# Optimization experiments

Hardware: AMD Instinct MI355X
Metric: run time of the kernel (lower is better)

The kernel has to match this reference:

```python
import jax, jax.numpy as jnp
import numpy as np

N, C, H, W = 16, 64, 128, 128
SHIFT = 1  # frozen value of torch module's random.randint(-2, 2) drawn at __init__


def setup_inputs() -> dict:
    key = jax.random.key(0)
    k1, k2, k3 = jax.random.split(key, 3)
    x = jax.random.normal(k1, (N, C, H, W), dtype=jnp.float32)
    # p_3: Conv2d(c, c, (1,5), padding=(0,2), bias=False) -> weight (C_out, C_in, 1, 5)
    w3 = jax.random.normal(k2, (C, C, 1, 5), dtype=jnp.float32) * (1.0 / np.sqrt(5.0 * C))
    # p_7: Conv2d(9c, c, 1, groups=c, bias=False) -> per output channel, 9 input channels: (C, 9)
    w7 = jax.random.normal(k3, (C, 9), dtype=jnp.float32) * (1.0 / 3.0)
    return {"x": x, "w3": w3, "w7": w7}


def reference(x, w3, w7):
    n, c, h, w = x.shape
    # t_1: F.unfold(x, (1,3), dilation=(1,2), padding=(0,2)) -> width offsets -2, 0, +2 (zero padded)
    xp = jnp.pad(x, ((0, 0), (0, 0), (0, 0), (2, 2)))
    t1 = jnp.stack([xp[..., 0:w], xp[..., 2:w + 2], xp[..., 4:w + 4]], axis=2)  # (n,c,3,h,w)
    # t_3: 1x5 conv, padding (0,2)
    t3 = jax.lax.conv_general_dilated(
        x, w3, window_strides=(1, 1), padding=[(0, 0), (2, 2)],
        dimension_numbers=("NCHW", "OIHW", "NCHW"))  # (n,c,h,w)
    # t_4: F.unfold(t1 as (n,3c,h,w), (3,1), padding=(1,0)) -> height offsets -1, 0, +1
    t1p = jnp.pad(t1, ((0, 0), (0, 0), (0, 0), (1, 1), (0, 0)))
    t4 = jnp.stack([t1p[..., 0:h, :], t1p[..., 1:h + 1, :], t1p[..., 2:h + 2, :]],
                   axis=3)  # (n, c, 3[w_off], 3[h_off], h, w)
    # t_5: roll along the W axis (dim 5)
    t5 = jnp.roll(t4, SHIFT, axis=5)
    # t_6: maximum of lhs (n,c,1,3,h,w) and rhs (n,c,3,3,h,w); lhs offset dim aligns with rhs dim 3
    t6 = jnp.maximum(t1[:, :, None, :, :, :], t5)  # (n,c,3,3,h,w)
    # t_7: grouped 1x1 conv, groups=c, 9 input channels per group -> 1 output channel
    t6f = t6.reshape(n, c, 9, h, w)
    t7 = jnp.einsum("nckhw,ck->nchw", t6f, w7)
    return t7 * t3
```

## Files before the change

### kernel.cpp

```cpp
#include <hip/hip_runtime.h>

#define NN 16
#define CC 64
#define HH 128
#define WW 128

#define LDS_STRIDE 72
#define PANEL_DW   4752
#define ROW_BYTES  19008
#define ROW_CHUNKS 1188
#define T3B_STRIDE 132

typedef __attribute__((ext_vector_type(8))) short short8;
typedef __attribute__((ext_vector_type(4))) float floatx4;

__device__ __forceinline__ short f2bf(float f) {
    union { float f; unsigned u; } v; v.f = f;
    unsigned r = v.u + 0x7fffu + ((v.u >> 16) & 1u);
    return (short)(r >> 16);
}
__device__ __forceinline__ unsigned pack2bf(float lo, float hi) {
    union { float f; unsigned u; } a, b; a.f = lo; b.f = hi;
    unsigned ra = a.u + 0x7fffu + ((a.u >> 16) & 1u);
    unsigned rb = b.u + 0x7fffu + ((b.u >> 16) & 1u);
    return (ra >> 16) | (rb & 0xffff0000u);
}
__device__ __forceinline__ float bf2f(unsigned short u) {
    union { unsigned u; float f; } v; v.u = ((unsigned)u) << 16;
    return v.f;
}
__device__ __forceinline__ void gload_lds16(const void* g, void* l) {
    __builtin_amdgcn_global_load_lds(
        (const __attribute__((address_space(1))) void*)g,
        (__attribute__((address_space(3))) void*)l, 16, 0, 0);
}

__global__ __launch_bounds__(256) void prep_w(const float* __restrict__ w3,
                                              short* __restrict__ Apk,
                                              float* __restrict__ zp) {
    int idx = blockIdx.x * 256 + threadIdx.x;
    if (idx < CC * 320) {
        int co = idx / 320;
        int kk = idx % 320;
        int mh = co >> 5, m = (co >> 4) & 1, lm = co & 15;
        int ks = kk >> 5, g = (kk >> 3) & 3, e = kk & 7;
        int tap = kk >> 6, ci = kk & 63;
        Apk[((((mh * 10 + ks) * 2 + m) * 64) + (g * 16 + lm)) * 8 + e] =
            f2bf(w3[(co * CC + ci) * 5 + tap]);
    }
    if (blockIdx.x == 0 && threadIdx.x < 64) zp[threadIdx.x] = 0.f;
}

__global__ __launch_bounds__(256, 4) void transp(const float* __restrict__ x,
                                                 short* __restrict__ xT) {
    __shared__ __align__(16) char smem[2 * ROW_BYTES];
    unsigned* xsW = (unsigned*)smem;

    const int bid = blockIdx.x;
    const int rp  = ((bid & 7) << 7) | (bid >> 3);
    const int n   = rp >> 6;
    const int h   = (rp & 63) * 2;
    const int tid = threadIdx.x;
    const int lane = tid & 63;
    const int W    = tid >> 6;

    {
        const int ri = lane >> 5;
        const int wq = lane & 31;
        unsigned* panel = xsW + ri * PANEL_DW;
        #pragma unroll
        for (int i = 0; i < 8; ++i) {
            const int cp = W * 8 + i;
            const float* b0 = x + (((size_t)(n * CC + 2 * cp)) * HH + h) * WW;
            float4 av = *(const float4*)(b0 + lane * 4);
            float4 bv = *(const float4*)(b0 + HH * WW + lane * 4);
            #pragma unroll
            for (int k = 0; k < 4; ++k) {
                int wp = wq * 4 + 2 + k;
                panel[wp * 36 + cp] = pack2bf(av[k], bv[k]);
            }
        }
        {
            int pi  = tid >> 7;
            int idx = tid & 127;
            int wpi = idx >> 5;
            int wpz = (wpi < 2) ? wpi : 128 + wpi;
            xsW[pi * PANEL_DW + wpz * 36 + (idx & 31)] = 0u;
        }
    }
    __syncthreads();

    const size_t rowb = (size_t)(n * HH + h) * ROW_BYTES;
    #pragma unroll
    for (int pi = 0; pi < 2; ++pi) {
        short8* dst = (short8*)((char*)xT + rowb + (size_t)pi * ROW_BYTES);
        const short8* src = (const short8*)(smem + pi * ROW_BYTES);
        #pragma unroll
        for (int i = 0; i < 5; ++i) {
            int c = tid + 256 * i;
            if (c < ROW_CHUNKS) dst[c] = src[c];
        }
    }
}

__global__ __launch_bounds__(256, 6) void fused(const short* __restrict__ xT,
                                                const short* __restrict__ Apk,
                                                const float* __restrict__ x,
                                                const float* __restrict__ w7,
                                                const float* __restrict__ zp,
                                                float* __restrict__ out) {
    __shared__ __align__(16) char smem[19456];
    const short* panel = (const short*)smem;
    short*       t3b  = (short*)smem;

    const int bid = blockIdx.x;
    const int nh  = ((bid & 7) << 8) | (bid >> 3);
    const int n   = nh >> 7;
    const int h   = nh & (HH - 1);
    const int tid = threadIdx.x;
    const int lane = tid & 63;
    const int W    = tid >> 6;

    {
        const char* grow = (const char*)xT + (size_t)(n * HH + h) * ROW_BYTES;
        #pragma unroll
        for (int k2 = 0; k2 < 5; ++k2) {
            int base = (k2 * 4 + W) * 1024;
            if (base < ROW_BYTES) {
                int goff = base + lane * 16;
                if (goff > ROW_BYTES - 16) goff = ROW_BYTES - 16;
                gload_lds16(grow + goff, smem + base);
            }
        }
    }
    __syncthreads();

    const int lm = lane & 15;
    const int g  = lane >> 4;
    const int mh = W >> 1;
    const int wh = W & 1;

    floatx4 acc[2][4];
    #pragma unroll
    for (int m = 0; m < 2; ++m)
        #pragma unroll
        for (int j = 0; j < 4; ++j) acc[m][j] = (floatx4){0.f, 0.f, 0.f, 0.f};

    for (int ks = 0; ks < 10; ++ks) {
        const int kbase = ks * 32 + g * 8;
        const int tap   = kbase >> 6;
        const int cib   = kbase & 63;

        const short* ab = Apk + (((mh * 10 + ks) * 2) * 64 + lane) * 8;
        short8 a0 = *(const short8*)ab;
        short8 a1 = *(const short8*)(ab + 64 * 8);
        #pragma unroll
        for (int j = 0; j < 4; ++j) {
            int wp = (wh * 4 + j) * 16 + lm + tap;
            short8 b = *(const short8*)&panel[wp * LDS_STRIDE + cib];
            acc[0][j] = __builtin_amdgcn_mfma_f32_16x16x32_bf16(a0, b, acc[0][j], 0, 0, 0);
            acc[1][j] = __builtin_amdgcn_mfma_f32_16x16x32_bf16(a1, b, acc[1][j], 0, 0, 0);
        }
    }
    __syncthreads();

    #pragma unroll
    for (int m = 0; m < 2; ++m)
        #pragma unroll
        for (int j = 0; j < 4; ++j)
            #pragma unroll
            for (int r = 0; r < 4; ++r) {
                int co = (mh * 2 + m) * 16 + g * 4 + r;
                int w  = (wh * 4 + j) * 16 + lm;
                t3b[co * T3B_STRIDE + w] = f2bf(acc[m][j][r]);
            }

    const int w0   = (tid & 31) * 4;
    const int chi  = tid >> 5;
    const int lq31 = lane & 31;
    const bool isw = (lq31 == 0);
    const bool ise = (lq31 == 31);
    const int src31 = lane | 31;
    const int lsrc  = isw ? lane : lane - 1;
    const int rsrc  = ise ? lane : lane + 1;

    const float* pr[3]; int sr[3];
    const float* xb0 = x + (((size_t)(n * CC + chi)) * HH) * WW;
    #pragma unroll
    for (int r = 0; r < 3; ++r) {
        int hh = h + r - 1;
        bool hok = (unsigned)hh < HH;
        pr[r] = hok ? (xb0 + (size_t)hh * WW + w0) : zp;
        sr[r] = hok ? (8 * HH * WW) : 0;
    }
    const float* wcp = w7 + chi * 9;
    int t3o = chi * T3B_STRIDE + w0;
    float* outp = out + ((((size_t)(n * CC + chi)) * HH + h) * WW) + w0;

    __syncthreads();

    #define BUILD_WIN(dst, c)                                              \
        {                                                                  \
            float l1_ = __shfl((c).y, lsrc);                               \
            float l2_ = __shfl((c).z, lsrc);                               \
            float l3_ = __shfl((c).w, lsrc);                               \
            float r8_ = __shfl((c).x, rsrc);                               \
            float r9_ = __shfl((c).y, rsrc);                               \
            dst[1] = isw ? 0.f : l1_;                                      \
            dst[2] = isw ? 0.f : l2_;                                      \
            dst[3] = isw ? 0.f : l3_;                                      \
            dst[4] = (c).x; dst[5] = (c).y; dst[6] = (c).z; dst[7] = (c).w;\
            dst[8] = ise ? 0.f : r8_;                                      \
            dst[9] = ise ? 0.f : r9_;                                      \
        }

    #pragma unroll
    for (int it = 0; it < 8; ++it) {
        float4 cur[3];
        #pragma unroll
        for (int r = 0; r < 3; ++r) { cur[r] = *(const float4*)pr[r]; pr[r] += sr[r]; }
        float wc[9];
        #pragma unroll
        for (int t = 0; t < 9; ++t) wc[t] = wcp[t];
        ushort4 tv = *(const ushort4*)&t3b[t3o];

        float wrap0[3], wrap1[3];
        #pragma unroll
        for (int r = 0; r < 3; ++r) {
            wrap0[r] = __shfl(cur[r].y, src31);
            wrap1[r] = __shfl(cur[r].w, src31);
        }

        float win1[12];
        BUILD_WIN(win1, cur[1]);

        float t3v[4] = {bf2f(tv.x), bf2f(tv.y), bf2f(tv.z), bf2f(tv.w)};

        float res[4] = {0.f, 0.f, 0.f, 0.f};
        #pragma unroll
        for (int i = 0; i < 3; ++i) {
            float wini[12];
            if (i == 1) {
                #pragma unroll
                for (int t = 1; t < 10; ++t) wini[t] = win1[t];
            } else {
                BUILD_WIN(wini, cur[i]);
            }
            #pragma unroll
            for (int j = 0; j < 3; ++j) {
                #pragma unroll
                for (int e = 0; e < 4; ++e) {
                    float lhs = win1[e + 2 * i + 2];
                    float rhs = wini[e + 2 * j + 1];
                    if (e == 0)
                        rhs = isw ? ((j == 0) ? wrap0[i]
                                   : (j == 1) ? wrap1[i] : 0.f)
                                  : rhs;
                    res[e] = fmaf(wc[j * 3 + i], fmaxf(lhs, rhs), res[e]);
                }
            }
        }
        float4 o;
        o.x = res[0] * t3v[0]; o.y = res[1] * t3v[1];
        o.z = res[2] * t3v[2]; o.w = res[3] * t3v[3];
        *(float4*)outp = o;

        wcp  += 8 * 9;
        t3o  += 8 * T3B_STRIDE;
        outp += (size_t)8 * HH * WW;
    }
    #undef BUILD_WIN
}

extern "C" void kernel_launch(void* const* d_in, const int* in_sizes, int n_in,
                              void* d_out, int out_size, void* d_ws, size_t ws_size,
                              hipStream_t stream) {
    const float* x  = (const float*)d_in[0];
    const float* w3 = (const float*)d_in[1];
    const float* w7 = (const float*)d_in[2];
    float* out = (float*)d_out;

    short* Apk = (short*)d_ws;
    float* zp  = (float*)((char*)d_ws + 40960);
    short* xT  = (short*)((char*)d_ws + 65536);

    prep_w<<<(CC * 320 + 255) / 256, 256, 0, stream>>>(w3, Apk, zp);
    transp<<<NN * HH / 2, 256, 0, stream>>>(x, xT);
    fused<<<NN * HH, 256, 0, stream>>>(xT, Apk, x, w7, zp, out);
}
```

Baseline: 148.1 us.

## Fuse bf16 transpose/pack into main kernel, dropping separate transpose pass

Removes the separate transpose kernel that wrote a bf16 channel-interleaved copy of x to workspace. The fused kernel now reads fp32 x directly for its row, packs channel pairs to bf16 and scatters them into the LDS panel with zero padding columns. This avoids a full write and re-read of the intermediate buffer and one kernel launch. In exchange, each block does uncoalesced-ish strided LDS scatter stores and fp32 global reads itself, and loses the async global-to-LDS load path.

```diff
diff --git a/kernel.cpp b/kernel.cpp
--- a/kernel.cpp
+++ b/kernel.cpp
@@ -6,9 +6,6 @@
 #define WW 128
 
 #define LDS_STRIDE 72
-#define PANEL_DW   4752
-#define ROW_BYTES  19008
-#define ROW_CHUNKS 1188
 #define T3B_STRIDE 132
 
 typedef __attribute__((ext_vector_type(8))) short short8;
@@ -28,11 +25,6 @@
 __device__ __forceinline__ float bf2f(unsigned short u) {
     union { unsigned u; float f; } v; v.u = ((unsigned)u) << 16;
     return v.f;
-}
-__device__ __forceinline__ void gload_lds16(const void* g, void* l) {
-    __builtin_amdgcn_global_load_lds(
-        (const __attribute__((address_space(1))) void*)g,
-        (__attribute__((address_space(3))) void*)l, 16, 0, 0);
 }
 
 __global__ __launch_bounds__(256) void prep_w(const float* __restrict__ w3,
@@ -51,65 +43,13 @@
     if (blockIdx.x == 0 && threadIdx.x < 64) zp[threadIdx.x] = 0.f;
 }
 
-__global__ __launch_bounds__(256, 4) void transp(const float* __restrict__ x,
-                                                 short* __restrict__ xT) {
-    __shared__ __align__(16) char smem[2 * ROW_BYTES];
-    unsigned* xsW = (unsigned*)smem;
-
-    const int bid = blockIdx.x;
-    const int rp  = ((bid & 7) << 7) | (bid >> 3);
-    const int n   = rp >> 6;
-    const int h   = (rp & 63) * 2;
-    const int tid = threadIdx.x;
-    const int lane = tid & 63;
-    const int W    = tid >> 6;
-
-    {
-        const int ri = lane >> 5;
-        const int wq = lane & 31;
-        unsigned* panel = xsW + ri * PANEL_DW;
-        #pragma unroll
-        for (int i = 0; i < 8; ++i) {
-            const int cp = W * 8 + i;
-            const float* b0 = x + (((size_t)(n * CC + 2 * cp)) * HH + h) * WW;
-            float4 av = *(const float4*)(b0 + lane * 4);
-            float4 bv = *(const float4*)(b0 + HH * WW + lane * 4);
-            #pragma unroll
-            for (int k = 0; k < 4; ++k) {
-                int wp = wq * 4 + 2 + k;
-                panel[wp * 36 + cp] = pack2bf(av[k], bv[k]);
-            }
-        }
-        {
-            int pi  = tid >> 7;
-            int idx = tid & 127;
-            int wpi = idx >> 5;
-            int wpz = (wpi < 2) ? wpi : 128 + wpi;
-            xsW[pi * PANEL_DW + wpz * 36 + (idx & 31)] = 0u;
-        }
-    }
-    __syncthreads();
-
-    const size_t rowb = (size_t)(n * HH + h) * ROW_BYTES;
-    #pragma unroll
-    for (int pi = 0; pi < 2; ++pi) {
-        short8* dst = (short8*)((char*)xT + rowb + (size_t)pi * ROW_BYTES);
-        const short8* src = (const short8*)(smem + pi * ROW_BYTES);
-        #pragma unroll
-        for (int i = 0; i < 5; ++i) {
-            int c = tid + 256 * i;
-            if (c < ROW_CHUNKS) dst[c] = src[c];
-        }
-    }
-}
-
-__global__ __launch_bounds__(256, 6) void fused(const short* __restrict__ xT,
-                                                const short* __restrict__ Apk,
+__global__ __launch_bounds__(256, 6) void fused(const short* __restrict__ Apk,
                                                 const float* __restrict__ x,
                                                 const float* __restrict__ w7,
                                                 const float* __restrict__ zp,
                                                 float* __restrict__ out) {
     __shared__ __align__(16) char smem[19456];
+    unsigned*    xsW  = (unsigned*)smem;
     const short* panel = (const short*)smem;
     short*       t3b  = (short*)smem;
 
@@ -122,15 +62,25 @@
     const int W    = tid >> 6;
 
     {
-        const char* grow = (const char*)xT + (size_t)(n * HH + h) * ROW_BYTES;
-        #pragma unroll
-        for (int k2 = 0; k2 < 5; ++k2) {
-            int base = (k2 * 4 + W) * 1024;
-            if (base < ROW_BYTES) {
-                int goff = base + lane * 16;
-                if (goff > ROW_BYTES - 16) goff = ROW_BYTES - 16;
-                gload_lds16(grow + goff, smem + base);
-            }
+        const int half = lane >> 5;
+        const int wq   = lane & 31;
+        const float* rowbase = x + ((size_t)n * CC * HH + h) * WW;
+        #pragma unroll
+        for (int i = 0; i < 4; ++i) {
+            const int cp = W * 8 + i * 2 + half;
+            const float* b0 = rowbase + (size_t)(2 * cp) * (HH * WW);
+            float4 av = *(const float4*)(b0 + wq * 4);
+            float4 bv = *(const float4*)(b0 + HH * WW + wq * 4);
+            #pragma unroll
+            for (int k = 0; k < 4; ++k) {
+                int wp = wq * 4 + 2 + k;
+                xsW[wp * 36 + cp] = pack2bf(av[k], bv[k]);
+            }
+        }
+        if (tid < 128) {
+            int wpi = tid >> 5;
+            int wpz = (wpi < 2) ? wpi : 128 + wpi;
+            xsW[wpz * 36 + (tid & 31)] = 0u;
         }
     }
     __syncthreads();
@@ -282,9 +232,7 @@
 
     short* Apk = (short*)d_ws;
     float* zp  = (float*)((char*)d_ws + 40960);
-    short* xT  = (short*)((char*)d_ws + 65536);
 
     prep_w<<<(CC * 320 + 255) / 256, 256, 0, stream>>>(w3, Apk, zp);
-    transp<<<NN * HH / 2, 256, 0, stream>>>(x, xT);
-    fused<<<NN * HH, 256, 0, stream>>>(xT, Apk, x, w7, zp, out);
-}
+    fused<<<NN * HH, 256, 0, stream>>>(Apk, x, w7, zp, out);
+}
```

Result: faster. 140.3 us (-5.3%).
